# Kernel optimization log

Hardware: AMD Instinct MI355X
Metric: run time of the kernel (lower is better)

## Reference

```python
import jax, jax.numpy as jnp
import numpy as np

EPS = 1e-5  # batchnorm eps (torch default)


def setup_inputs() -> dict:
    key = jax.random.key(0)
    ks = jax.random.split(key, 16)
    N, E, Din, H, Dout = 100000, 600000, 128, 128, 64
    x = jax.random.normal(ks[0], (N, Din), dtype=jnp.float32)
    edge_index = jax.random.randint(ks[1], (2, E), 0, N, dtype=jnp.int64)
    def lin(k, fan_in, fan_out):
        s = 1.0 / np.sqrt(fan_in)
        return jax.random.uniform(k, (fan_in, fan_out), jnp.float32, -s, s)
    return {
        "x": x,
        "edge_index": edge_index,
        "W1": lin(ks[2], Din, H), "b1": jnp.zeros((H,), jnp.float32),
        "W2": lin(ks[3], H, H),   "b2": jnp.zeros((H,), jnp.float32),
        "W3": lin(ks[4], H, H),   "b3": jnp.zeros((H,), jnp.float32),
        "W4": lin(ks[5], H, Dout),"b4": jnp.zeros((Dout,), jnp.float32),
        "g1": jnp.ones((H,), jnp.float32), "be1": jnp.zeros((H,), jnp.float32),
        "g2": jnp.ones((H,), jnp.float32), "be2": jnp.zeros((H,), jnp.float32),
        "g3": jnp.ones((H,), jnp.float32), "be3": jnp.zeros((H,), jnp.float32),
    }


def _gcn_norm(edge_index, N, dtype):
    # GCNConv default: add self-loops, symmetric normalization D^-1/2 A D^-1/2
    loop = jnp.arange(N, dtype=edge_index.dtype)
    src = jnp.concatenate([edge_index[0], loop])
    dst = jnp.concatenate([edge_index[1], loop])
    deg = jax.ops.segment_sum(jnp.ones_like(src, dtype=dtype), dst, num_segments=N)
    dinv = jax.lax.rsqrt(deg)  # deg >= 1 thanks to self-loops
    norm = dinv[src] * dinv[dst]  # [E+N]
    return src, dst, norm


def _conv(h, W, b, src, dst, norm, N):
    hw = h @ W                      # [N, out]
    msg = hw[src] * norm[:, None]   # gather + scale, [E+N, out]
    return jax.ops.segment_sum(msg, dst, num_segments=N) + b


def _bn(h, gamma, beta):
    # training-mode batchnorm over node dimension (biased variance)
    mu = jnp.mean(h, axis=0)
    var = jnp.mean(jnp.square(h - mu), axis=0)
    return (h - mu) * jax.lax.rsqrt(var + EPS) * gamma + beta


def reference(x, edge_index, W1, b1, W2, b2, W3, b3, W4, b4,
              g1, be1, g2, be2, g3, be3):
    N = x.shape[0]
    src, dst, norm = _gcn_norm(edge_index, N, x.dtype)
    h = jax.nn.relu(_conv(x, W1, b1, src, dst, norm, N))
    h = _bn(h, g1, be1)
    h = jax.nn.relu(_conv(h, W2, b2, src, dst, norm, N))
    h = _bn(h, g2, be2)
    h = jax.nn.relu(_conv(h, W3, b3, src, dst, norm, N))
    h = _bn(h, g3, be3)
    h = jax.nn.relu(_conv(h, W4, b4, src, dst, norm, N))
    return h
```

## Files before the change

### kernel.cpp

```cpp
#include <hip/hip_runtime.h>

#define BN_EPS 1e-5f

using bfrag = __attribute__((ext_vector_type(8))) short;
using f32x4 = __attribute__((ext_vector_type(4))) float;

__device__ inline float bf2f(unsigned int h16) {
    union { unsigned int u; float f; } v; v.u = h16 << 16; return v.f;
}
__device__ inline unsigned short f2bf(float f) {
    union { float f; unsigned int u; } v; v.f = f;
    unsigned int u = v.u;
    u += 0x7fffu + ((u >> 16) & 1u);
    return (unsigned short)(u >> 16);
}
__device__ inline void unpack8(uint4 u, float* f) {
    f[0] = bf2f(u.x & 0xffffu); f[1] = bf2f(u.x >> 16);
    f[2] = bf2f(u.y & 0xffffu); f[3] = bf2f(u.y >> 16);
    f[4] = bf2f(u.z & 0xffffu); f[5] = bf2f(u.z >> 16);
    f[6] = bf2f(u.w & 0xffffu); f[7] = bf2f(u.w >> 16);
}
__device__ inline void fma8(uint4 G, float w, float* acc) {
    float v[8];
    unpack8(G, v);
#pragma unroll
    for (int k = 0; k < 8; ++k) acc[k] += w * v[k];
}


__global__ void count_kernel(const int* __restrict__ ei, int E, int* __restrict__ cnt) {
    int e = blockIdx.x * blockDim.x + threadIdx.x;
    if (e < E) atomicAdd(&cnt[ei[E + e]], 1);
}

__global__ void dinv_kernel(const int* __restrict__ cnt, float* __restrict__ dinv, int N) {
    int i = blockIdx.x * blockDim.x + threadIdx.x;
    if (i < N) dinv[i] = rsqrtf((float)(cnt[i] + 1));
}

__global__ __launch_bounds__(1024) void scan_blocks(const int* __restrict__ cnt,
                                                    int* __restrict__ rowptr,
                                                    int* __restrict__ bsum, int N) {
    __shared__ int sh[1024];
    int t = threadIdx.x;
    int i = blockIdx.x * 1024 + t;
    int v = (i < N) ? cnt[i] : 0;
    sh[t] = v;
    __syncthreads();
    for (int off = 1; off < 1024; off <<= 1) {
        int x = (t >= off) ? sh[t - off] : 0;
        __syncthreads();
        sh[t] += x;
        __syncthreads();
    }
    if (i < N) rowptr[i] = sh[t] - v;
    if (t == 1023) bsum[blockIdx.x] = sh[1023];
}

__global__ void scan_carry(const int* __restrict__ bsum, int* __restrict__ boff, int nblk) {
    if (threadIdx.x == 0 && blockIdx.x == 0) {
        int run = 0;
        for (int b = 0; b < nblk; ++b) { int v = bsum[b]; boff[b] = run; run += v; }
        boff[nblk] = run;
    }
}

__global__ void scan_add(int* __restrict__ rowptr, const int* __restrict__ boff,
                         int* __restrict__ cursor, int N, int nblk) {
    int i = blockIdx.x * blockDim.x + threadIdx.x;
    if (i < N) {
        int v = rowptr[i] + boff[i >> 10];
        rowptr[i] = v;
        cursor[i] = v;
    }
    if (i == 0) rowptr[N] = boff[nblk];
}

__global__ void fill_kernel(const int* __restrict__ ei, int E, int* __restrict__ cursor,
                            const float* __restrict__ dinv, int2* __restrict__ epack) {
    int e = blockIdx.x * blockDim.x + threadIdx.x;
    if (e < E) {
        int s = ei[e], d = ei[E + e];
        int p = atomicAdd(&cursor[d], 1);
        float nrm = dinv[s] * dinv[d];
        epack[p] = make_int2(s, __float_as_int(nrm));
    }
}

__global__ void s_kernel(const int* __restrict__ rowptr, const int2* __restrict__ epack,
                         const float* __restrict__ dinv, float* __restrict__ sarr, int N) {
    int i = blockIdx.x * blockDim.x + threadIdx.x;
    if (i < N) {
        float a = dinv[i] * dinv[i];
        int j1 = rowptr[i + 1];
        for (int j = rowptr[i]; j < j1; ++j) a += __int_as_float(epack[j].y);
        sarr[i] = a;
    }
}


template <bool HASBN>
__global__ __launch_bounds__(256) void prep_kernel(const float* __restrict__ W, int COLS,
                                                   const float* __restrict__ stats,
                                                   const float* __restrict__ g,
                                                   const float* __restrict__ be, float invN,
                                                   unsigned short* __restrict__ Wt,
                                                   float* __restrict__ cvec) {
    __shared__ float sc[128], sh[128];
    int tid = threadIdx.x;
    if (tid < 128) {
        if (HASBN) {
            float mu  = stats[tid] * invN;
            float var = stats[128 + tid] * invN - mu * mu;
            float rs  = rsqrtf(var + BN_EPS);
            float s   = rs * g[tid];
            sc[tid] = s;
            sh[tid] = be[tid] - mu * s;
        } else { sc[tid] = 1.f; sh[tid] = 0.f; }
    }
    __syncthreads();
    int total = 128 * COLS;
    for (int idx = blockIdx.x * 256 + tid; idx < total; idx += gridDim.x * 256) {
        int k = idx / COLS, j = idx % COLS;
        Wt[j * 128 + k] = f2bf(sc[k] * W[idx]);
    }
    if (blockIdx.x == 0 && tid < COLS) {
        float a = 0.f;
        if (HASBN)
            for (int k = 0; k < 128; ++k) a += sh[k] * W[k * COLS + tid];
        cvec[tid] = a;
    }
}


template <int COLS, bool IN_F32>
__global__ __launch_bounds__(256) void gemm_mfma(const void* __restrict__ Hin,
                                                 const unsigned short* __restrict__ Wt,
                                                 unsigned short* __restrict__ out, int N) {
    __shared__ unsigned short Hs[64][136];
    const int tid  = threadIdx.x;
    const int row0 = blockIdx.x * 64;

    if (IN_F32) {
        const float* H = (const float*)Hin;
#pragma unroll
        for (int it = 0; it < 8; ++it) {
            int idx = it * 256 + tid;
            int r = idx >> 5, c4 = (idx & 31) * 4;
            float4 v = {0.f, 0.f, 0.f, 0.f};
            if (row0 + r < N) v = *(const float4*)(H + (size_t)(row0 + r) * 128 + c4);
            Hs[r][c4 + 0] = f2bf(v.x); Hs[r][c4 + 1] = f2bf(v.y);
            Hs[r][c4 + 2] = f2bf(v.z); Hs[r][c4 + 3] = f2bf(v.w);
        }
    } else {
        const unsigned short* H = (const unsigned short*)Hin;
#pragma unroll
        for (int it = 0; it < 4; ++it) {
            int idx = it * 256 + tid;
            int r = idx >> 4, c8 = (idx & 15) * 8;
            uint4 v = {0u, 0u, 0u, 0u};
            if (row0 + r < N) v = *(const uint4*)(H + (size_t)(row0 + r) * 128 + c8);
            *(uint4*)&Hs[r][c8] = v;
        }
    }
    __syncthreads();

    const int lane = tid & 63, wave = tid >> 6;
    const int arow = lane & 15, kg = lane >> 4;
    const int r0   = wave * 16;

    bfrag af[4];
#pragma unroll
    for (int kc = 0; kc < 4; ++kc) af[kc] = *(const bfrag*)&Hs[r0 + arow][kc * 32 + kg * 8];

    constexpr int NT = COLS / 16;
    f32x4 acc[NT];
#pragma unroll
    for (int nt = 0; nt < NT; ++nt) acc[nt] = (f32x4){0.f, 0.f, 0.f, 0.f};

#pragma unroll
    for (int nt = 0; nt < NT; ++nt) {
        const unsigned short* wp = Wt + (size_t)(nt * 16 + arow) * 128 + kg * 8;
#pragma unroll
        for (int kc = 0; kc < 4; ++kc) {
            bfrag bf = *(const bfrag*)(wp + kc * 32);
            acc[nt] = __builtin_amdgcn_mfma_f32_16x16x32_bf16(af[kc], bf, acc[nt], 0, 0, 0);
        }
    }
    __syncthreads();

#pragma unroll
    for (int nt = 0; nt < NT; ++nt) {
        int col = nt * 16 + arow;
#pragma unroll
        for (int r = 0; r < 4; ++r)
            Hs[r0 + kg * 4 + r][col] = f2bf(acc[nt][r]);
    }
    __syncthreads();

    constexpr int CH = COLS / 8;
    for (int idx = tid; idx < 64 * CH; idx += 256) {
        int r = idx / CH, c8 = (idx % CH) * 8;
        if (row0 + r < N)
            *(uint4*)(out + (size_t)(row0 + r) * COLS + c8) = *(const uint4*)&Hs[r][c8];
    }
}


template <int F, bool STATS, bool HASC, typename TOUT>
__global__ __launch_bounds__(256) void agg_kernel(const unsigned short* __restrict__ HW,
                                                  const int* __restrict__ rowptr,
                                                  const int2* __restrict__ epack,
                                                  const float* __restrict__ dinv,
                                                  const float* __restrict__ sarr,
                                                  const float* __restrict__ cvec,
                                                  const float* __restrict__ bias,
                                                  TOUT* __restrict__ out,
                                                  float* __restrict__ stats, int N) {
    constexpr int TPR = F / 8;
    constexpr int RPB = 256 / TPR;
    const int tid = threadIdx.x;
    const int lr  = tid / TPR;
    const int j8  = (tid % TPR) * 8;

    float ssum[8], ssq[8];
    if (STATS) {
#pragma unroll
        for (int k = 0; k < 8; ++k) { ssum[k] = 0.f; ssq[k] = 0.f; }
    }

#define LOADE(G, w, ii)                                            \
    do { int _i = (ii);                                            \
        if (_i < j1) { int2 _e = epack[_i];                        \
            w = __int_as_float(_e.y);                              \
            G = *(const uint4*)(HW + (size_t)_e.x * F + j8); }     \
    } while (0)
#define CONS(G, w, ii)                                             \
    do { if ((ii) < j1) fma8(G, w, acc); } while (0)

    for (int base = blockIdx.x * RPB; base < N; base += gridDim.x * RPB) {
        int row = base + lr;
        if (row >= N) continue;

        const int j0 = rowptr[row];
        const int j1 = rowptr[row + 1];

        uint4 u = *(const uint4*)(HW + (size_t)row * F + j8);

        uint4 A0, A1, A2, A3, B0, B1, B2, B3;
        float wa0, wa1, wa2, wa3, wb0, wb1, wb2, wb3;
        LOADE(A0, wa0, j0 + 0);
        LOADE(A1, wa1, j0 + 1);
        LOADE(A2, wa2, j0 + 2);
        LOADE(A3, wa3, j0 + 3);

        float di = dinv[row];
        float w0 = di * di;
        float acc[8];
        {
            float v[8];
            unpack8(u, v);
#pragma unroll
            for (int k = 0; k < 8; ++k) acc[k] = w0 * v[k];
        }

        for (int b = j0; b < j1; b += 8) {
            LOADE(B0, wb0, b + 4);
            LOADE(B1, wb1, b + 5);
            LOADE(B2, wb2, b + 6);
            LOADE(B3, wb3, b + 7);
            CONS(A0, wa0, b + 0);
            CONS(A1, wa1, b + 1);
            CONS(A2, wa2, b + 2);
            CONS(A3, wa3, b + 3);
            LOADE(A0, wa0, b + 8);
            LOADE(A1, wa1, b + 9);
            LOADE(A2, wa2, b + 10);
            LOADE(A3, wa3, b + 11);
            CONS(B0, wb0, b + 4);
            CONS(B1, wb1, b + 5);
            CONS(B2, wb2, b + 6);
            CONS(B3, wb3, b + 7);
        }

        if (HASC) {
            float sv = sarr[row];
#pragma unroll
            for (int k = 0; k < 8; ++k) acc[k] += cvec[j8 + k] * sv;
        }
#pragma unroll
        for (int k = 0; k < 8; ++k) acc[k] = fmaxf(acc[k] + bias[j8 + k], 0.f);

        if constexpr (sizeof(TOUT) == 2) {
            unsigned int w0b = (unsigned int)f2bf(acc[0]) | ((unsigned int)f2bf(acc[1]) << 16);
            unsigned int w1b = (unsigned int)f2bf(acc[2]) | ((unsigned int)f2bf(acc[3]) << 16);
            unsigned int w2b = (unsigned int)f2bf(acc[4]) | ((unsigned int)f2bf(acc[5]) << 16);
            unsigned int w3b = (unsigned int)f2bf(acc[6]) | ((unsigned int)f2bf(acc[7]) << 16);
            uint4 o = {w0b, w1b, w2b, w3b};
            *(uint4*)((unsigned short*)out + (size_t)row * F + j8) = o;
        } else {
            float4 o0 = {acc[0], acc[1], acc[2], acc[3]};
            float4 o1 = {acc[4], acc[5], acc[6], acc[7]};
            *(float4*)((float*)out + (size_t)row * F + j8)     = o0;
            *(float4*)((float*)out + (size_t)row * F + j8 + 4) = o1;
        }
        if (STATS) {
#pragma unroll
            for (int k = 0; k < 8; ++k) {
                ssum[k] += acc[k];
                ssq[k]  += acc[k] * acc[k];
            }
        }
    }
#undef LOADE
#undef CONS

    if constexpr (STATS) {
        __shared__ float red[RPB][F];
#pragma unroll
        for (int k = 0; k < 8; ++k) red[lr][j8 + k] = ssum[k];
        __syncthreads();
        if (tid < F) {
            float a = 0.f;
#pragma unroll
            for (int r = 0; r < RPB; ++r) a += red[r][tid];
            atomicAdd(&stats[tid], a);
        }
        __syncthreads();
#pragma unroll
        for (int k = 0; k < 8; ++k) red[lr][j8 + k] = ssq[k];
        __syncthreads();
        if (tid < F) {
            float a = 0.f;
#pragma unroll
            for (int r = 0; r < RPB; ++r) a += red[r][tid];
            atomicAdd(&stats[F + tid], a);
        }
    }
}


extern "C" void kernel_launch(void* const* d_in, const int* in_sizes, int n_in,
                              void* d_out, int out_size, void* d_ws, size_t ws_size,
                              hipStream_t stream) {
    const float* x  = (const float*)d_in[0];
    const int*   ei = (const int*)d_in[1];
    const float* W1 = (const float*)d_in[2];  const float* b1 = (const float*)d_in[3];
    const float* W2 = (const float*)d_in[4];  const float* b2 = (const float*)d_in[5];
    const float* W3 = (const float*)d_in[6];  const float* b3 = (const float*)d_in[7];
    const float* W4 = (const float*)d_in[8];  const float* b4 = (const float*)d_in[9];
    const float* g1 = (const float*)d_in[10]; const float* be1 = (const float*)d_in[11];
    const float* g2 = (const float*)d_in[12]; const float* be2 = (const float*)d_in[13];
    const float* g3 = (const float*)d_in[14]; const float* be3 = (const float*)d_in[15];

    const int N = in_sizes[0] / 128;
    const int E = in_sizes[1] / 2;
    const int nblk = (N + 1023) / 1024;

    size_t off = 0;
    char* ws = (char*)d_ws;
    auto alloc = [&](size_t bytes) -> void* {
        void* p = ws + off;
        off += (bytes + 255) & ~(size_t)255;
        return p;
    };
    int*   cnt    = (int*)alloc((size_t)N * 4);
    float* dinv   = (float*)alloc((size_t)N * 4);
    int*   rowptr = (int*)alloc((size_t)(N + 1) * 4);
    int*   cursor = (int*)alloc((size_t)N * 4);
    int*   bsum   = (int*)alloc((size_t)nblk * 4);
    int*   boff   = (int*)alloc((size_t)(nblk + 1) * 4);
    int2*  epack  = (int2*)alloc((size_t)E * 8);
    float* sarr   = (float*)alloc((size_t)N * 4);
    float* stats  = (float*)alloc(256 * 4);
    unsigned short* Wt = (unsigned short*)alloc(128 * 128 * 2);
    float* cvec   = (float*)alloc(128 * 4);
    unsigned short* hA  = (unsigned short*)alloc((size_t)N * 128 * 2);
    unsigned short* hwB = (unsigned short*)alloc((size_t)N * 128 * 2);
    (void)ws_size; (void)n_in; (void)out_size;

    const int TB = 256;
    const int gE = (E + TB - 1) / TB;
    const int gN = (N + TB - 1) / TB;

    hipMemsetAsync(cnt, 0, (size_t)N * 4, stream);
    count_kernel<<<gE, TB, 0, stream>>>(ei, E, cnt);
    dinv_kernel<<<gN, TB, 0, stream>>>(cnt, dinv, N);
    scan_blocks<<<nblk, 1024, 0, stream>>>(cnt, rowptr, bsum, N);
    scan_carry<<<1, 1, 0, stream>>>(bsum, boff, nblk);
    scan_add<<<gN, TB, 0, stream>>>(rowptr, boff, cursor, N, nblk);
    fill_kernel<<<gE, TB, 0, stream>>>(ei, E, cursor, dinv, epack);
    s_kernel<<<gN, TB, 0, stream>>>(rowptr, epack, dinv, sarr, N);

    const int gG  = (N + 63) / 64;
    const int gA  = 2048;
    const float invN = 1.0f / (float)N;

    prep_kernel<false><<<8, 256, 0, stream>>>(W1, 128, nullptr, nullptr, nullptr, 0.f, Wt, cvec);
    gemm_mfma<128, true><<<gG, 256, 0, stream>>>(x, Wt, hwB, N);
    hipMemsetAsync(stats, 0, 256 * 4, stream);
    agg_kernel<128, true, false, unsigned short><<<gA, 256, 0, stream>>>(
        hwB, rowptr, epack, dinv, sarr, cvec, b1, hA, stats, N);

    prep_kernel<true><<<8, 256, 0, stream>>>(W2, 128, stats, g1, be1, invN, Wt, cvec);
    gemm_mfma<128, false><<<gG, 256, 0, stream>>>(hA, Wt, hwB, N);
    hipMemsetAsync(stats, 0, 256 * 4, stream);
    agg_kernel<128, true, true, unsigned short><<<gA, 256, 0, stream>>>(
        hwB, rowptr, epack, dinv, sarr, cvec, b2, hA, stats, N);

    prep_kernel<true><<<8, 256, 0, stream>>>(W3, 128, stats, g2, be2, invN, Wt, cvec);
    gemm_mfma<128, false><<<gG, 256, 0, stream>>>(hA, Wt, hwB, N);
    hipMemsetAsync(stats, 0, 256 * 4, stream);
    agg_kernel<128, true, true, unsigned short><<<gA, 256, 0, stream>>>(
        hwB, rowptr, epack, dinv, sarr, cvec, b3, hA, stats, N);

    prep_kernel<true><<<8, 256, 0, stream>>>(W4, 64, stats, g3, be3, invN, Wt, cvec);
    gemm_mfma<64, false><<<gG, 256, 0, stream>>>(hA, Wt, hwB, N);
    agg_kernel<64, false, true, float><<<gA, 256, 0, stream>>>(
        hwB, rowptr, epack, dinv, sarr, cvec, b4, (float*)d_out, nullptr, N);
}
```

Before: 491.3 us.

## Stage per-block edge records in LDS and launch one block per row group

The aggregation kernel drops its grid-stride loop and launches one block per group of 16 (or 32) rows. Each block first copies the contiguous range of packed edge records for its rows into shared memory, up to 1024 entries, and falls back to global memory past that cap. The goal is to stop the threads sharing a row from each re-reading the same edge index/weight records from global memory. The cost is many more blocks, a sync before any gathers start, and no latency hiding across row iterations within a block.

Result: slower. 760.2 us (+54.7%).

```diff
diff --git a/kernel.cpp b/kernel.cpp
--- a/kernel.cpp
+++ b/kernel.cpp
@@ -219,9 +219,19 @@
                                                   float* __restrict__ stats, int N) {
     constexpr int TPR = F / 8;
     constexpr int RPB = 256 / TPR;
-    const int tid = threadIdx.x;
-    const int lr  = tid / TPR;
-    const int j8  = (tid % TPR) * 8;
+    constexpr int CAP = 1024;
+    __shared__ int2 eld[CAP];
+
+    const int tid  = threadIdx.x;
+    const int lr   = tid / TPR;
+    const int j8   = (tid % TPR) * 8;
+    const int base = blockIdx.x * RPB;
+
+    const int e0     = rowptr[base];
+    const int eend   = rowptr[min(base + RPB, N)];
+    const int estage = min(eend - e0, CAP);
+    for (int i = tid; i < estage; i += 256) eld[i] = epack[e0 + i];
+    __syncthreads();
 
     float ssum[8], ssq[8];
     if (STATS) {
@@ -229,23 +239,20 @@
         for (int k = 0; k < 8; ++k) { ssum[k] = 0.f; ssq[k] = 0.f; }
     }
 
-#define LOADE(G, w, ii)                                            \
-    do { int _i = (ii);                                            \
-        if (_i < j1) { int2 _e = epack[_i];                        \
+    const int row = base + lr;
+    if (row < N) {
+        const int j0 = rowptr[row] - e0;
+        const int j1 = rowptr[row + 1] - e0;
+
+#define REC(jj) ((jj) < CAP ? eld[jj] : epack[e0 + (jj)])
+#define LOADE(G, w, jj)                                            \
+    do { int _j = (jj);                                            \
+        if (_j < j1) { int2 _e = REC(_j);                          \
             w = __int_as_float(_e.y);                              \
             G = *(const uint4*)(HW + (size_t)_e.x * F + j8); }     \
     } while (0)
-#define CONS(G, w, ii)                                             \
-    do { if ((ii) < j1) fma8(G, w, acc); } while (0)
-
-    for (int base = blockIdx.x * RPB; base < N; base += gridDim.x * RPB) {
-        int row = base + lr;
-        if (row >= N) continue;
-
-        const int j0 = rowptr[row];
-        const int j1 = rowptr[row + 1];
-
-        uint4 u = *(const uint4*)(HW + (size_t)row * F + j8);
+#define CONS(G, w, jj)                                             \
+    do { if ((jj) < j1) fma8(G, w, acc); } while (0)
 
         uint4 A0, A1, A2, A3, B0, B1, B2, B3;
         float wa0, wa1, wa2, wa3, wb0, wb1, wb2, wb3;
@@ -254,6 +261,7 @@
         LOADE(A2, wa2, j0 + 2);
         LOADE(A3, wa3, j0 + 3);
 
+        uint4 u = *(const uint4*)(HW + (size_t)row * F + j8);
         float di = dinv[row];
         float w0 = di * di;
         float acc[8];
@@ -282,6 +290,9 @@
             CONS(B2, wb2, b + 6);
             CONS(B3, wb3, b + 7);
         }
+#undef REC
+#undef LOADE
+#undef CONS
 
         if (HASC) {
             float sv = sarr[row];
@@ -312,8 +323,6 @@
             }
         }
     }
-#undef LOADE
-#undef CONS
 
     if constexpr (STATS) {
         __shared__ float red[RPB][F];
@@ -392,30 +401,31 @@
     fill_kernel<<<gE, TB, 0, stream>>>(ei, E, cursor, dinv, epack);
     s_kernel<<<gN, TB, 0, stream>>>(rowptr, epack, dinv, sarr, N);
 
-    const int gG  = (N + 63) / 64;
-    const int gA  = 2048;
+    const int gG   = (N + 63) / 64;
+    const int gA16 = (N + 15) / 16;
+    const int gA32 = (N + 31) / 32;
     const float invN = 1.0f / (float)N;
 
     prep_kernel<false><<<8, 256, 0, stream>>>(W1, 128, nullptr, nullptr, nullptr, 0.f, Wt, cvec);
     gemm_mfma<128, true><<<gG, 256, 0, stream>>>(x, Wt, hwB, N);
     hipMemsetAsync(stats, 0, 256 * 4, stream);
-    agg_kernel<128, true, false, unsigned short><<<gA, 256, 0, stream>>>(
+    agg_kernel<128, true, false, unsigned short><<<gA16, 256, 0, stream>>>(
         hwB, rowptr, epack, dinv, sarr, cvec, b1, hA, stats, N);
 
     prep_kernel<true><<<8, 256, 0, stream>>>(W2, 128, stats, g1, be1, invN, Wt, cvec);
     gemm_mfma<128, false><<<gG, 256, 0, stream>>>(hA, Wt, hwB, N);
     hipMemsetAsync(stats, 0, 256 * 4, stream);
-    agg_kernel<128, true, true, unsigned short><<<gA, 256, 0, stream>>>(
+    agg_kernel<128, true, true, unsigned short><<<gA16, 256, 0, stream>>>(
         hwB, rowptr, epack, dinv, sarr, cvec, b2, hA, stats, N);
 
     prep_kernel<true><<<8, 256, 0, stream>>>(W3, 128, stats, g2, be2, invN, Wt, cvec);
     gemm_mfma<128, false><<<gG, 256, 0, stream>>>(hA, Wt, hwB, N);
     hipMemsetAsync(stats, 0, 256 * 4, stream);
-    agg_kernel<128, true, true, unsigned short><<<gA, 256, 0, stream>>>(
+    agg_kernel<128, true, true, unsigned short><<<gA16, 256, 0, stream>>>(
         hwB, rowptr, epack, dinv, sarr, cvec, b3, hA, stats, N);
 
     prep_kernel<true><<<8, 256, 0, stream>>>(W4, 64, stats, g3, be3, invN, Wt, cvec);
     gemm_mfma<64, false><<<gG, 256, 0, stream>>>(hA, Wt, hwB, N);
-    agg_kernel<64, false, true, float><<<gA, 256, 0, stream>>>(
+    agg_kernel<64, false, true, float><<<gA32, 256, 0, stream>>>(
         hwB, rowptr, epack, dinv, sarr, cvec, b4, (float*)d_out, nullptr, N);
 }
```
